# Performance work log

Measured on AMD Instinct MI355X. Metric: run time of the kernel, lower is better.

## Reference

```python
import jax, jax.numpy as jnp
import numpy as np

CMIN, CMAX = -1024.0, 1016.0  # clamp(min=-2**10, max=2**10 - 8) after every op
BRIGHT_F = 1.9   # 1.0 + linspace(0, 0.9, 11)[10]
COLOR_F = 1.9    # 1.0 + linspace(0, 0.9, 11)[10]


def _brightness_dct(x, f):
    # pixel-domain multiplicative brightness; DCT is linear -> scale all coeffs
    return x * f


def _contrast_dct(x, f):
    # pixel contrast: (p - mean)*f + mean.
    # In DCT: AC coeffs scale by f; DC coeff blends toward per-channel mean DC.
    dc_mean = jnp.mean(x[..., 0, 0], axis=(-2, -1), keepdims=True)  # [C,1,1]
    out = x * f
    out = out.at[..., 0, 0].add((1.0 - f) * dc_mean)
    return out


def setup_inputs() -> dict:
    key = jax.random.key(0)
    k1, k2 = jax.random.split(key)
    # luma: [C=1, Hblocks, Wblocks, 8, 8]; chroma 4:2:0: [C=2, H/2, W/2, 8, 8]
    y = jax.random.normal(k1, (1, 512, 512, 8, 8), dtype=jnp.float32) * 100.0
    c = jax.random.normal(k2, (2, 256, 256, 8, 8), dtype=jnp.float32) * 100.0
    return {"y": y, "c": c}


def reference(y, c):
    clamp = lambda t: jnp.clip(t, CMIN, CMAX)
    # dct_prep(mode='start') treated as identity; initial clamp as in forward()
    y = clamp(y)
    c = clamp(c)
    # op 1: Brightness on luma (coeff[0]); both planes clamped after each op
    y = clamp(_brightness_dct(y, BRIGHT_F))
    c = clamp(c)
    # op 2: Color = contrast on chroma (coeff[1])
    c = clamp(_contrast_dct(c, COLOR_F))
    y = clamp(y)
    # dct_prep(mode='end') treated as identity
    return y, c
```

## Files before the change

kernel.cpp:

```cpp
#include <hip/hip_runtime.h>

#define CMIN -1024.0f
#define CMAX 1016.0f

__device__ __forceinline__ float clampv(float x) {
    return fminf(fmaxf(x, CMIN), CMAX);
}

__device__ __forceinline__ float wave_reduce(float v) {
    #pragma unroll
    for (int off = 32; off > 0; off >>= 1)
        v += __shfl_down(v, off, 64);
    return v;
}


__global__ void __launch_bounds__(256)
payload_kernel(const float4* __restrict__ y4, const float4* __restrict__ c4,
               float4* __restrict__ out, float* __restrict__ partials,
               float* __restrict__ dcbuf, int ynvec, int yblocks)
{
    const int tid = blockIdx.x * blockDim.x + threadIdx.x;

    if (tid < ynvec) {
        float4 v = y4[tid];
        v.x = clampv(clampv(v.x) * 1.9f);
        v.y = clampv(clampv(v.y) * 1.9f);
        v.z = clampv(clampv(v.z) * 1.9f);
        v.w = clampv(clampv(v.w) * 1.9f);
        out[tid] = v;
    } else {
        const int ic = tid - ynvec;
        float4 v = c4[ic];
        float4 r;
        r.x = clampv(v.x) * 1.9f;
        r.y = clampv(v.y) * 1.9f;
        r.z = clampv(v.z) * 1.9f;
        r.w = clampv(v.w) * 1.9f;

        float dcv = 0.0f;
        if ((ic & 15) == 0) {
            dcv = clampv(v.x);
            dcbuf[ic >> 4] = r.x;
        }
        r.x = clampv(r.x);
        r.y = clampv(r.y);
        r.z = clampv(r.z);
        r.w = clampv(r.w);
        out[tid] = r;

        __shared__ float smem[4];
        float s = wave_reduce(dcv);
        const int lane = threadIdx.x & 63;
        const int wave = threadIdx.x >> 6;
        if (lane == 0) smem[wave] = s;
        __syncthreads();
        if (threadIdx.x == 0)
            partials[blockIdx.x - yblocks] = smem[0] + smem[1] + smem[2] + smem[3];
    }
}

__global__ void __launch_bounds__(256)
dc_fixup(float* __restrict__ outf, const float* __restrict__ partials,
         const float* __restrict__ dcbuf, int dc_per_ch,
         float neg09_inv_count)
{
    const int d = blockIdx.x * blockDim.x + threadIdx.x;

    const float pre = dcbuf[d];

    float s0 = 0.0f, s1 = 0.0f;
    for (int j = threadIdx.x; j < 4096; j += 256) {
        s0 += partials[j];
        s1 += partials[4096 + j];
    }
    s0 = wave_reduce(s0);
    s1 = wave_reduce(s1);

    __shared__ float sm[8];
    __shared__ float sadj[2];
    const int lane = threadIdx.x & 63;
    const int wave = threadIdx.x >> 6;
    if (lane == 0) { sm[wave] = s0; sm[4 + wave] = s1; }
    __syncthreads();
    if (threadIdx.x == 0) {
        sadj[0] = (sm[0] + sm[1] + sm[2] + sm[3]) * neg09_inv_count;
        sadj[1] = (sm[4] + sm[5] + sm[6] + sm[7]) * neg09_inv_count;
    }
    __syncthreads();

    const float adj = (d < dc_per_ch) ? sadj[0] : sadj[1];
    outf[(size_t)d * 64] = clampv(pre + adj);
}

extern "C" void kernel_launch(void* const* d_in, const int* in_sizes, int n_in,
                              void* d_out, int out_size, void* d_ws, size_t ws_size,
                              hipStream_t stream) {
    const float* y = (const float*)d_in[0];
    const float* c = (const float*)d_in[1];
    float* out = (float*)d_out;
    float* ws  = (float*)d_ws;

    const int yN = in_sizes[0];
    const int cN = in_sizes[1];

    const int ynvec    = yN / 4;
    const int cnvec    = cN / 4;
    const int yblocks  = ynvec / 256;
    const int cblocks  = cnvec / 256;
    const int dc_count = cN / 64;
    const int dc_per_ch = dc_count / 2;
    const float neg09_inv_count = -0.9f / (float)dc_per_ch;

    float* partials = ws;
    float* dcbuf    = ws + 8192;

    payload_kernel<<<yblocks + cblocks, 256, 0, stream>>>(
        (const float4*)y, (const float4*)c, (float4*)out, partials, dcbuf,
        ynvec, yblocks);

    dc_fixup<<<dc_count / 256, 256, 0, stream>>>(
        out + (size_t)yN, partials, dcbuf, dc_per_ch, neg09_inv_count);
}
```

Before: 180.8 us.

## Fuse DC fixup into payload kernel using sentinel-tagged partials and spin-wait

Merges the two launches into one. Each chroma block publishes its partial DC sum, tagged with a sentinel in the upper 32 bits, through an atomic 64-bit store. The last 512 chroma blocks spin until all 8192 partials are present, then reduce them and write the corrected DC coefficients, recomputing each pre-value from the input. This removes the second kernel launch and the dcbuf round-trip. In exchange it relies on forward-progress assumptions: waiting blocks could deadlock if producer blocks never get scheduled. The sentinel is also never cleared, so stale workspace left from a previous call could be read as valid.

```diff
diff --git a/kernel.cpp b/kernel.cpp
--- a/kernel.cpp
+++ b/kernel.cpp
@@ -2,6 +2,7 @@
 
 #define CMIN -1024.0f
 #define CMAX 1016.0f
+#define SENTINEL 0x13572468u
 
 __device__ __forceinline__ float clampv(float x) {
     return fminf(fmaxf(x, CMIN), CMAX);
@@ -14,73 +15,91 @@
     return v;
 }
 
+__global__ void __launch_bounds__(256)
+fused_all(const float4* __restrict__ y4, const float4* __restrict__ c4,
+          const float* __restrict__ cf, float4* __restrict__ out,
+          unsigned long long* __restrict__ pairs,
+          int ynvec, int yblocks, int cblocks, int dc_per_ch,
+          float neg09_inv_count)
+{
+    __shared__ float sm[8];
+    __shared__ float sadj[2];
 
-__global__ void __launch_bounds__(256)
-payload_kernel(const float4* __restrict__ y4, const float4* __restrict__ c4,
-               float4* __restrict__ out, float* __restrict__ partials,
-               float* __restrict__ dcbuf, int ynvec, int yblocks)
-{
-    const int tid = blockIdx.x * blockDim.x + threadIdx.x;
+    const int bid = blockIdx.x;
+    const int tid = bid * 256 + threadIdx.x;
+    const int lane = threadIdx.x & 63;
+    const int wave = threadIdx.x >> 6;
 
-    if (tid < ynvec) {
+    if (bid < yblocks) {
         float4 v = y4[tid];
         v.x = clampv(clampv(v.x) * 1.9f);
         v.y = clampv(clampv(v.y) * 1.9f);
         v.z = clampv(clampv(v.z) * 1.9f);
         v.w = clampv(clampv(v.w) * 1.9f);
         out[tid] = v;
+        return;
+    }
+
+    const int cb = bid - yblocks;
+    const int ic = tid - ynvec;
+    float4 v = c4[ic];
+    const bool isDC = (ic & 15) == 0;
+
+    float ry = clampv(clampv(v.y) * 1.9f);
+    float rz = clampv(clampv(v.z) * 1.9f);
+    float rw = clampv(clampv(v.w) * 1.9f);
+    if (!isDC) {
+        float4 r;
+        r.x = clampv(clampv(v.x) * 1.9f);
+        r.y = ry; r.z = rz; r.w = rw;
+        out[ynvec + ic] = r;
     } else {
-        const int ic = tid - ynvec;
-        float4 v = c4[ic];
-        float4 r;
-        r.x = clampv(v.x) * 1.9f;
-        r.y = clampv(v.y) * 1.9f;
-        r.z = clampv(v.z) * 1.9f;
-        r.w = clampv(v.w) * 1.9f;
+        float* p = (float*)&out[ynvec + ic];
+        p[1] = ry; p[2] = rz; p[3] = rw;
+    }
 
-        float dcv = 0.0f;
-        if ((ic & 15) == 0) {
-            dcv = clampv(v.x);
-            dcbuf[ic >> 4] = r.x;
+    float dcv = isDC ? clampv(v.x) : 0.0f;
+    float s = wave_reduce(dcv);
+    if (lane == 0) sm[wave] = s;
+    __syncthreads();
+    if (threadIdx.x == 0) {
+        float part = sm[0] + sm[1] + sm[2] + sm[3];
+        unsigned long long pk =
+            ((unsigned long long)SENTINEL << 32) | (unsigned long long)__float_as_uint(part);
+        __hip_atomic_store(&pairs[cb], pk, __ATOMIC_RELAXED,
+                           __HIP_MEMORY_SCOPE_AGENT);
+    }
+
+    const int fb = cb - (cblocks - 512);
+    if (fb < 0) return;
+    __syncthreads();
+
+    unsigned long long pk[32];
+    #pragma unroll
+    for (int k = 0; k < 32; ++k)
+        pk[k] = __hip_atomic_load(&pairs[threadIdx.x + (k << 8)],
+                                  __ATOMIC_RELAXED, __HIP_MEMORY_SCOPE_AGENT);
+    for (;;) {
+        bool all = true;
+        #pragma unroll
+        for (int k = 0; k < 32; ++k) {
+            if ((unsigned)(pk[k] >> 32) != SENTINEL) {
+                all = false;
+                pk[k] = __hip_atomic_load(&pairs[threadIdx.x + (k << 8)],
+                                          __ATOMIC_RELAXED,
+                                          __HIP_MEMORY_SCOPE_AGENT);
+            }
         }
-        r.x = clampv(r.x);
-        r.y = clampv(r.y);
-        r.z = clampv(r.z);
-        r.w = clampv(r.w);
-        out[tid] = r;
-
-        __shared__ float smem[4];
-        float s = wave_reduce(dcv);
-        const int lane = threadIdx.x & 63;
-        const int wave = threadIdx.x >> 6;
-        if (lane == 0) smem[wave] = s;
-        __syncthreads();
-        if (threadIdx.x == 0)
-            partials[blockIdx.x - yblocks] = smem[0] + smem[1] + smem[2] + smem[3];
+        if (all) break;
     }
-}
-
-__global__ void __launch_bounds__(256)
-dc_fixup(float* __restrict__ outf, const float* __restrict__ partials,
-         const float* __restrict__ dcbuf, int dc_per_ch,
-         float neg09_inv_count)
-{
-    const int d = blockIdx.x * blockDim.x + threadIdx.x;
-
-    const float pre = dcbuf[d];
 
     float s0 = 0.0f, s1 = 0.0f;
-    for (int j = threadIdx.x; j < 4096; j += 256) {
-        s0 += partials[j];
-        s1 += partials[4096 + j];
-    }
+    #pragma unroll
+    for (int k = 0; k < 16; ++k) s0 += __uint_as_float((unsigned)pk[k]);
+    #pragma unroll
+    for (int k = 16; k < 32; ++k) s1 += __uint_as_float((unsigned)pk[k]);
     s0 = wave_reduce(s0);
     s1 = wave_reduce(s1);
-
-    __shared__ float sm[8];
-    __shared__ float sadj[2];
-    const int lane = threadIdx.x & 63;
-    const int wave = threadIdx.x >> 6;
     if (lane == 0) { sm[wave] = s0; sm[4 + wave] = s1; }
     __syncthreads();
     if (threadIdx.x == 0) {
@@ -89,8 +108,10 @@
     }
     __syncthreads();
 
+    const int d = fb * 256 + threadIdx.x;
     const float adj = (d < dc_per_ch) ? sadj[0] : sadj[1];
-    outf[(size_t)d * 64] = clampv(pre + adj);
+    const float pre = clampv(cf[(size_t)d * 64]) * 1.9f;
+    ((float*)&out[ynvec])[(size_t)d * 64] = clampv(pre + adj);
 }
 
 extern "C" void kernel_launch(void* const* d_in, const int* in_sizes, int n_in,
@@ -99,7 +120,6 @@
     const float* y = (const float*)d_in[0];
     const float* c = (const float*)d_in[1];
     float* out = (float*)d_out;
-    float* ws  = (float*)d_ws;
 
     const int yN = in_sizes[0];
     const int cN = in_sizes[1];
@@ -108,17 +128,11 @@
     const int cnvec    = cN / 4;
     const int yblocks  = ynvec / 256;
     const int cblocks  = cnvec / 256;
-    const int dc_count = cN / 64;
-    const int dc_per_ch = dc_count / 2;
+    const int dc_per_ch = (cN / 64) / 2;
     const float neg09_inv_count = -0.9f / (float)dc_per_ch;
 
-    float* partials = ws;
-    float* dcbuf    = ws + 8192;
-
-    payload_kernel<<<yblocks + cblocks, 256, 0, stream>>>(
-        (const float4*)y, (const float4*)c, (float4*)out, partials, dcbuf,
-        ynvec, yblocks);
-
-    dc_fixup<<<dc_count / 256, 256, 0, stream>>>(
-        out + (size_t)yN, partials, dcbuf, dc_per_ch, neg09_inv_count);
+    fused_all<<<yblocks + cblocks, 256, 0, stream>>>(
+        (const float4*)y, (const float4*)c, c, (float4*)out,
+        (unsigned long long*)d_ws, ynvec, yblocks, cblocks, dc_per_ch,
+        neg09_inv_count);
 }
```

Result: slower. 187.7 us (+3.8%).
